# Optimization experiments

Measured on AMD Instinct MI355X. Metric: run time of the kernel, lower is better.

Reference implementation:

```python
import jax, jax.numpy as jnp
import numpy as np

DIM = 2048
N_HEADS = 32
N_KV_HEADS = 8
HEAD_DIM = 64
N_REP = N_HEADS // N_KV_HEADS
SEQ = 2048
BATCH = 1


def _llama3_scaled_rope(head_dim, end, base=10000.0, scale_factor=8):
    # matches executorch precompute_freqs_cis with use_scaled=True
    freqs = 1.0 / (base ** (np.arange(0, head_dim, 2)[: head_dim // 2] / head_dim))
    low_freq_factor, high_freq_factor, old_ctx = 1.0, 4.0, 8192.0
    low_wl = old_ctx / low_freq_factor
    high_wl = old_ctx / high_freq_factor
    wavelen = 2.0 * np.pi / freqs
    smooth = (old_ctx / wavelen - low_freq_factor) / (high_freq_factor - low_freq_factor)
    scaled = np.where(
        wavelen < high_wl,
        freqs,
        np.where(wavelen > low_wl, freqs / scale_factor,
                 (1.0 - smooth) * freqs / scale_factor + smooth * freqs),
    )
    t = np.arange(end, dtype=np.float64)
    ang = np.outer(t, scaled)
    return np.cos(ang).astype(np.float32), np.sin(ang).astype(np.float32)


def setup_inputs() -> dict:
    key = jax.random.key(0)
    kx, kq, kk, kv, ko = jax.random.split(key, 5)
    x = jax.random.normal(kx, (BATCH, SEQ, DIM), dtype=jnp.float32)
    sc = 0.02
    wq = jax.random.normal(kq, (N_HEADS * HEAD_DIM, DIM), dtype=jnp.float32) * sc
    wk = jax.random.normal(kk, (N_KV_HEADS * HEAD_DIM, DIM), dtype=jnp.float32) * sc
    wv = jax.random.normal(kv, (N_KV_HEADS * HEAD_DIM, DIM), dtype=jnp.float32) * sc
    wo = jax.random.normal(ko, (N_HEADS * HEAD_DIM, DIM), dtype=jnp.float32).T * sc
    cos, sin = _llama3_scaled_rope(HEAD_DIM, SEQ)
    return {"x": x, "freqs_cos": jnp.asarray(cos), "freqs_sin": jnp.asarray(sin),
            "wq": wq, "wk": wk, "wv": wv, "wo": wo}


def _apply_rotary(x, cos, sin):
    # x: [b, s, h, hd]; cos/sin: [s, hd//2]; interleaved-pair RoPE
    xr = x[..., 0::2]
    xi = x[..., 1::2]
    c = cos[None, :, None, :]
    s = sin[None, :, None, :]
    out_r = xr * c - xi * s
    out_i = xr * s + xi * c
    return jnp.stack([out_r, out_i], axis=-1).reshape(x.shape)


def reference(x, freqs_cos, freqs_sin, wq, wk, wv, wo):
    b, s, _ = x.shape
    q = (x @ wq.T).reshape(b, s, N_HEADS, HEAD_DIM)
    k = (x @ wk.T).reshape(b, s, N_KV_HEADS, HEAD_DIM)
    v = (x @ wv.T).reshape(b, s, N_KV_HEADS, HEAD_DIM)
    q = _apply_rotary(q, freqs_cos, freqs_sin)
    k = _apply_rotary(k, freqs_cos, freqs_sin)
    # [b, h, s, hd]
    q = q.transpose(0, 2, 1, 3)
    k = k.transpose(0, 2, 1, 3)
    v = v.transpose(0, 2, 1, 3)
    # GQA: repeat_interleave over head dim
    k = jnp.repeat(k, N_REP, axis=1)
    v = jnp.repeat(v, N_REP, axis=1)
    scale = 1.0 / jnp.sqrt(jnp.asarray(HEAD_DIM, dtype=x.dtype))
    scores = jnp.einsum("bhqd,bhkd->bhqk", q, k) * scale
    causal = jnp.tril(jnp.ones((s, s), dtype=bool))
    scores = jnp.where(causal[None, None], scores, jnp.finfo(scores.dtype).min)
    attn = jax.nn.softmax(scores, axis=-1)
    y = jnp.einsum("bhqk,bhkd->bhqd", attn, v)
    y = y.transpose(0, 2, 1, 3).reshape(b, s, N_HEADS * HEAD_DIM)
    return y @ wo.T
```

## Files before the change

kernel.cpp:

```cpp
#include <hip/hip_runtime.h>
#include <hip/hip_bf16.h>

typedef __attribute__((ext_vector_type(8))) __bf16 bf16x8;
typedef __attribute__((ext_vector_type(4))) __bf16 bf16x4;
typedef __attribute__((ext_vector_type(4))) float f32x4;
typedef __attribute__((ext_vector_type(16))) float f32x16;

#define DIM 2048
#define SEQ 2048
#define NH 32
#define NKV 8
#define HD 64
#define QKVD 3072
#define KOFF 2048
#define VOFF 2560
#define KVDIM 512

__device__ __forceinline__ void gld16(const __bf16* g, __bf16* l) {
    __builtin_amdgcn_global_load_lds(
        (const __attribute__((address_space(1))) void*)g,
        (__attribute__((address_space(3))) void*)l, 16, 0, 0);
}

__global__ __launch_bounds__(256) void cvt_all(const float* __restrict__ x,
                                               const float* __restrict__ wq,
                                               const float* __restrict__ wk,
                                               const float* __restrict__ wv,
                                               const float* __restrict__ wo,
                                               __bf16* __restrict__ xb,
                                               __bf16* __restrict__ wqkvb,
                                               __bf16* __restrict__ wob) {
    const int i = blockIdx.x * blockDim.x + threadIdx.x;
    const int NX = SEQ * DIM / 4;
    const int NW = DIM * DIM / 4;
    const int NKV4 = KVDIM * DIM / 4;
    const float* src; __bf16* dst; int off;
    if (i < NX)                        { src = x;  dst = xb;    off = i; }
    else if (i < NX + NW)              { src = wq; dst = wqkvb; off = i - NX; }
    else if (i < NX + NW + NKV4)       { src = wk; dst = wqkvb + (size_t)KOFF * DIM; off = i - NX - NW; }
    else if (i < NX + NW + 2 * NKV4)   { src = wv; dst = wqkvb + (size_t)VOFF * DIM; off = i - NX - NW - NKV4; }
    else                               { src = wo; dst = wob;   off = i - NX - NW - 2 * NKV4; }
    float4 v = reinterpret_cast<const float4*>(src)[off];
    bf16x4 o;
    o[0] = (__bf16)v.x; o[1] = (__bf16)v.y; o[2] = (__bf16)v.z; o[3] = (__bf16)v.w;
    reinterpret_cast<bf16x4*>(dst)[off] = o;
}

template <typename OutT, bool ROPE>
__global__ __launch_bounds__(512, 6) void gemm_tn(const __bf16* __restrict__ A,
                                                  const __bf16* __restrict__ B,
                                                  OutT* __restrict__ C,
                                                  int M, int N, int K,
                                                  float scale, int scaleNlim,
                                                  const float* __restrict__ fc,
                                                  const float* __restrict__ fs,
                                                  __bf16* __restrict__ VTout) {
    __shared__ __align__(16) __bf16 As[2][2][128 * 32];
    __shared__ __align__(16) __bf16 Bs[2][2][64 * 32];
    const int tid = threadIdx.x;
    const int lane = tid & 63;
    const int w = tid >> 6;
    const int l15 = lane & 15, lhi = lane >> 4;
    const int mb = blockIdx.y * 128;
    const int nb = blockIdx.x * 64;
    const int wm = (w >> 1) * 32, wn = (w & 1) * 32;

    const int srow = lane >> 2, scol = (lane & 3) * 8;
    const __bf16* gA = A + (size_t)(mb + w * 16 + srow) * K + scol;
    const __bf16* gB = B + (size_t)(nb + (w & 3) * 16 + srow) * K + scol;
    const int bsub = w >> 2;

    auto stage = [&](int kk, int buf) {
#pragma unroll
        for (int s = 0; s < 2; ++s)
            gld16(gA + kk + s * 32, As[buf][s] + w * 512);
        gld16(gB + kk + bsub * 32, Bs[buf][bsub] + (w & 3) * 512);
    };

    stage(0, 0);
    __syncthreads();

    f32x4 acc[2][2] = {};
    int cur = 0;
    for (int kk = 0; kk < K; kk += 64, cur ^= 1) {
        if (kk + 64 < K) stage(kk + 64, cur ^ 1);
#pragma unroll
        for (int s = 0; s < 2; ++s) {
            bf16x8 a[2], b[2];
#pragma unroll
            for (int i = 0; i < 2; ++i)
                a[i] = *reinterpret_cast<const bf16x8*>(&As[cur][s][(wm + i * 16 + l15) * 32 + lhi * 8]);
#pragma unroll
            for (int j = 0; j < 2; ++j)
                b[j] = *reinterpret_cast<const bf16x8*>(&Bs[cur][s][(wn + j * 16 + l15) * 32 + lhi * 8]);
#pragma unroll
            for (int i = 0; i < 2; ++i)
#pragma unroll
                for (int j = 0; j < 2; ++j)
                    acc[i][j] = __builtin_amdgcn_mfma_f32_16x16x32_bf16(a[i], b[j], acc[i][j], 0, 0, 0);
        }
        __syncthreads();
    }

    const bool toVT = ROPE && (VTout != nullptr) && (nb >= VOFF);
    if (toVT) {
#pragma unroll
        for (int i = 0; i < 2; ++i)
#pragma unroll
            for (int j = 0; j < 2; ++j) {
                bf16x4 pv;
#pragma unroll
                for (int r = 0; r < 4; ++r) pv[r] = (__bf16)acc[i][j][r];
                const int colv = nb - VOFF + wn + j * 16 + l15;
                const int row0 = mb + wm + i * 16 + lhi * 4;
                *reinterpret_cast<bf16x4*>(VTout + (size_t)colv * M + row0) = pv;
            }
    } else {
        const float sc = (nb < scaleNlim) ? scale : 1.0f;
        const bool doRope = ROPE && (nb < VOFF);
#pragma unroll
        for (int i = 0; i < 2; ++i)
#pragma unroll
            for (int j = 0; j < 2; ++j)
#pragma unroll
                for (int r = 0; r < 4; ++r) {
                    float v = acc[i][j][r] * sc;
                    if (doRope) {
                        const int col = nb + wn + j * 16 + l15;
                        const int row = mb + wm + i * 16 + lhi * 4 + r;
                        const float vp = __shfl_xor(v, 1);
                        const int fi = (col & 63) >> 1;
                        const float cc = fc[row * 32 + fi];
                        const float ss = fs[row * 32 + fi];
                        v = (col & 1) ? (vp * ss + v * cc) : (v * cc - vp * ss);
                    }
                    C[(size_t)(mb + wm + i * 16 + lhi * 4 + r) * N + nb + wn + j * 16 + l15] = (OutT)v;
                }
    }
}

__global__ __launch_bounds__(256, 4) void attn_kernel(const __bf16* __restrict__ QKV,
                                                      const __bf16* __restrict__ VT,
                                                      __bf16* __restrict__ Y) {
    const int bx = blockIdx.x;
    const int g = bx >> 8;
    const int a = (bx >> 5) & 7;
    const int h = bx & 31;
    const int qt = (g == 0) ? 31 - a : (g == 1) ? a : (g == 2) ? 23 - a : 8 + a;
    const int kvh = h >> 2;
    const int tid = threadIdx.x;
    const int lane = tid & 63;
    const int w = tid >> 6;
    const int l31 = lane & 31;
    const int lhi2 = lane >> 5;
    const int qhalf = w & 1;
    const int kvhalf = w >> 1;

    __shared__ __align__(16) unsigned char smem[40960];
    __bf16* Kl = (__bf16*)smem;
    __bf16* Vl = (__bf16*)(smem + 16384);
    __bf16* Pl = (__bf16*)(smem + 32768);

    const __bf16* Qp = QKV + h * HD;
    const __bf16* Kp = QKV + KOFF + kvh * HD;
    const __bf16* Vth = VT + (size_t)(kvh * HD) * SEQ;

    const int sr = lane >> 3;
    const int ksc = ((lane & 7) ^ sr) * 8;

    auto stage = [&](int jt, int buf) {
        const int kvb = jt * 64;
#pragma unroll
        for (int c = 0; c < 2; ++c) {
            const int row = w * 16 + c * 8;
            gld16(Kp + (size_t)(kvb + row + sr) * QKVD + ksc, Kl + buf * 4096 + row * 64);
            gld16(Vth + (size_t)(row + sr) * SEQ + kvb + ksc, Vl + buf * 4096 + row * 64);
        }
    };

    const int qb = qt * 64;
    const int qrow = qb + qhalf * 32 + l31;

    const __bf16* qptr = Qp + (size_t)qrow * QKVD;
    bf16x8 qf[4];
#pragma unroll
    for (int c = 0; c < 4; ++c)
        qf[c] = *reinterpret_cast<const bf16x8*>(qptr + c * 16 + lhi2 * 8);

    f32x16 o0 = {}, o1 = {};
    float mrun = -1e30f;
    float lpart = 0.f;

    const int pswz = l31 & 3;
    const int rsw7 = l31 & 7;

    stage(0, 0);
    __syncthreads();

    int cur = 0;
    for (int j = 0; j <= qt; ++j, cur ^= 1) {
        const bool pre = (j < qt);
        if (pre) stage(j + 1, cur ^ 1);

        if (!(j == qt && kvhalf == 1 && qhalf == 0)) {
            f32x16 sacc = {};
            const __bf16* Kb = Kl + cur * 4096 + (kvhalf * 32 + l31) * 64;
            __builtin_amdgcn_s_setprio(1);
#pragma unroll
            for (int c = 0; c < 4; ++c) {
                bf16x8 kf = *reinterpret_cast<const bf16x8*>(
                    Kb + (((c * 2 + lhi2) ^ rsw7) * 8));
                sacc = __builtin_amdgcn_mfma_f32_32x32x16_bf16(kf, qf[c], sacc, 0, 0, 0);
            }
            __builtin_amdgcn_s_setprio(0);

            if (j == qt && kvhalf == qhalf) {
#pragma unroll
                for (int r = 0; r < 16; ++r) {
                    const int kvl = (r & 3) + 8 * (r >> 2) + 4 * lhi2;
                    if (kvl > l31) sacc[r] = -1e30f;
                }
            }

            float pm = sacc[0];
#pragma unroll
            for (int r = 1; r < 16; ++r) pm = fmaxf(pm, sacc[r]);

            if (!__all(pm - mrun <= 8.0f)) {
                const float full = fmaxf(pm, __shfl_xor(pm, 32));
                const float mn = fmaxf(mrun, full);
                const float aa = exp2f(mrun - mn);
                mrun = mn;
                lpart *= aa;
#pragma unroll
                for (int r = 0; r < 16; ++r) {
                    const int qi = (r & 3) + 8 * (r >> 2) + 4 * lhi2;
                    const float ar = __shfl(aa, qi);
                    o0[r] *= ar; o1[r] *= ar;
                }
            }

            __bf16* Pw = Pl + w * 1024 + l31 * 32;
            float ps = 0.f;
#pragma unroll
            for (int gg = 0; gg < 4; ++gg) {
                bf16x4 pk;
#pragma unroll
                for (int rr = 0; rr < 4; ++rr) {
                    const float pv = exp2f(sacc[gg * 4 + rr] - mrun);
                    ps += pv;
                    pk[rr] = (__bf16)pv;
                }
                *reinterpret_cast<bf16x4*>(Pw + ((gg ^ pswz) * 8) + lhi2 * 4) = pk;
            }
            lpart += ps;

            bf16x8 pf[2];
#pragma unroll
            for (int c = 0; c < 2; ++c)
                pf[c] = *reinterpret_cast<const bf16x8*>(
                    Pw + (((c * 2 + lhi2) ^ pswz) * 8));
            const __bf16* Vb0 = Vl + cur * 4096 + l31 * 64;
            const __bf16* Vb1 = Vl + cur * 4096 + (32 + l31) * 64;
            __builtin_amdgcn_s_setprio(1);
#pragma unroll
            for (int c = 0; c < 2; ++c) {
                const int s = kvhalf * 4 + c * 2 + lhi2;
                bf16x8 vf0 = *reinterpret_cast<const bf16x8*>(Vb0 + ((s ^ rsw7) * 8));
                bf16x8 vf1 = *reinterpret_cast<const bf16x8*>(Vb1 + ((s ^ rsw7) * 8));
                o0 = __builtin_amdgcn_mfma_f32_32x32x16_bf16(pf[c], vf0, o0, 0, 0, 0);
                o1 = __builtin_amdgcn_mfma_f32_32x32x16_bf16(pf[c], vf1, o1, 0, 0, 0);
            }
            __builtin_amdgcn_s_setprio(0);
        }

        __syncthreads();
    }

    const float ls = lpart + __shfl_xor(lpart, 32);
    float* ex = (float*)smem;
    float* exm = (float*)(smem + 32768);

    if (kvhalf == 1) {
        float* dst = ex + qhalf * 2048 + lane * 32;
#pragma unroll
        for (int r = 0; r < 16; ++r) { dst[r] = o0[r]; dst[16 + r] = o1[r]; }
        if (lane < 32) {
            exm[qhalf * 64 + l31] = mrun;
            exm[qhalf * 64 + 32 + l31] = ls;
        }
    }
    __syncthreads();
    if (kvhalf == 0) {
        const float mo = exm[qhalf * 64 + l31];
        const float lso = exm[qhalf * 64 + 32 + l31];
        const float mn = fmaxf(mrun, mo);
        const float a0 = exp2f(mrun - mn);
        const float a1 = exp2f(mo - mn);
        const float lst = ls * a0 + lso * a1;
        const float* src = ex + qhalf * 2048 + lane * 32;
#pragma unroll
        for (int r = 0; r < 16; ++r) {
            const int qi = (r & 3) + 8 * (r >> 2) + 4 * lhi2;
            const float A0 = __shfl(a0, qi);
            const float A1 = __shfl(a1, qi);
            const float L = __shfl(lst, qi);
            const float v0 = (o0[r] * A0 + src[r] * A1) / L;
            const float v1 = (o1[r] * A0 + src[16 + r] * A1) / L;
            const size_t qg = (size_t)(qb + qhalf * 32 + qi);
            Y[qg * DIM + h * HD + l31] = (__bf16)v0;
            Y[qg * DIM + h * HD + 32 + l31] = (__bf16)v1;
        }
    }
}

extern "C" void kernel_launch(void* const* d_in, const int* in_sizes, int n_in,
                              void* d_out, int out_size, void* d_ws, size_t ws_size,
                              hipStream_t stream) {
    const float* x    = (const float*)d_in[0];
    const float* fcos = (const float*)d_in[1];
    const float* fsin = (const float*)d_in[2];
    const float* wq   = (const float*)d_in[3];
    const float* wk   = (const float*)d_in[4];
    const float* wv   = (const float*)d_in[5];
    const float* wo   = (const float*)d_in[6];
    float* out = (float*)d_out;

    __bf16* xb    = (__bf16*)d_ws;
    __bf16* wqkvb = xb + (size_t)SEQ * DIM;
    __bf16* wob   = wqkvb + (size_t)QKVD * DIM;
    __bf16* QKVb  = wob + (size_t)DIM * DIM;
    __bf16* Yb    = QKVb + (size_t)SEQ * QKVD;
    __bf16* VTb   = Yb + (size_t)SEQ * DIM;

    const int ncvt = (SEQ * DIM / 4) + 2 * (DIM * DIM / 4) + 2 * (KVDIM * DIM / 4);
    cvt_all<<<ncvt / 256, 256, 0, stream>>>(x, wq, wk, wv, wo, xb, wqkvb, wob);

    gemm_tn<__bf16, true><<<dim3(QKVD / 64, SEQ / 128), 512, 0, stream>>>(
        xb, wqkvb, QKVb, SEQ, QKVD, DIM, 0.125f * 1.4426950408889634f, KOFF,
        fcos, fsin, VTb);

    attn_kernel<<<dim3(1024), 256, 0, stream>>>(QKVb, VTb, Yb);

    gemm_tn<float, false><<<dim3(DIM / 64, SEQ / 128), 512, 0, stream>>>(
        Yb, wob, out, SEQ, DIM, DIM, 1.0f, 0, nullptr, nullptr, nullptr);
}
```

Baseline: 132.2 us.

## Process two query tiles per attention block and keep P in registers via permlane swap

The attention kernel now runs 512 threads per block covering two adjacent 64-row query tiles, so each staged K/V tile is shared by twice as many waves and the grid is halved. The PV MFMA operands are swapped so the probability fragment can be built in registers with packed bf16 conversion and permlane32_swap instead of a round trip through LDS. This drops per-row rescale shuffles and vectorizes the output stores. The cost is more threads per block, uneven causal work between the two tiles, and a changed block-to-tile mapping for load balance.

```diff
diff --git a/kernel.cpp b/kernel.cpp
--- a/kernel.cpp
+++ b/kernel.cpp
@@ -5,6 +5,7 @@
 typedef __attribute__((ext_vector_type(4))) __bf16 bf16x4;
 typedef __attribute__((ext_vector_type(4))) float f32x4;
 typedef __attribute__((ext_vector_type(16))) float f32x16;
+typedef __attribute__((ext_vector_type(4))) unsigned u32x4;
 
 #define DIM 2048
 #define SEQ 2048
@@ -20,6 +21,12 @@
     __builtin_amdgcn_global_load_lds(
         (const __attribute__((address_space(1))) void*)g,
         (__attribute__((address_space(3))) void*)l, 16, 0, 0);
+}
+
+__device__ __forceinline__ unsigned cvtpk(float lo, float hi) {
+    unsigned r;
+    asm("v_cvt_pk_bf16_f32 %0, %1, %2" : "=v"(r) : "v"(lo), "v"(hi));
+    return r;
 }
 
 __global__ __launch_bounds__(256) void cvt_all(const float* __restrict__ x,
@@ -139,27 +146,26 @@
     }
 }
 
-__global__ __launch_bounds__(256, 4) void attn_kernel(const __bf16* __restrict__ QKV,
+__global__ __launch_bounds__(512, 4) void attn_kernel(const __bf16* __restrict__ QKV,
                                                       const __bf16* __restrict__ VT,
                                                       __bf16* __restrict__ Y) {
     const int bx = blockIdx.x;
     const int g = bx >> 8;
     const int a = (bx >> 5) & 7;
     const int h = bx & 31;
-    const int qt = (g == 0) ? 31 - a : (g == 1) ? a : (g == 2) ? 23 - a : 8 + a;
+    const int p = g ? a : 15 - a;
     const int kvh = h >> 2;
     const int tid = threadIdx.x;
     const int lane = tid & 63;
     const int w = tid >> 6;
+    const int qtl = w >> 2, qhalf = w & 1, kvhalf = (w >> 1) & 1;
     const int l31 = lane & 31;
     const int lhi2 = lane >> 5;
-    const int qhalf = w & 1;
-    const int kvhalf = w >> 1;
-
-    __shared__ __align__(16) unsigned char smem[40960];
-    __bf16* Kl = (__bf16*)smem;
-    __bf16* Vl = (__bf16*)(smem + 16384);
-    __bf16* Pl = (__bf16*)(smem + 32768);
+
+    __shared__ __align__(16) __bf16 Kl[2][64 * 64];
+    __shared__ __align__(16) __bf16 Vl[2][64 * 64];
+    __shared__ float ex[4][64][32];
+    __shared__ float exm[4][2][32];
 
     const __bf16* Qp = QKV + h * HD;
     const __bf16* Kp = QKV + KOFF + kvh * HD;
@@ -170,16 +176,12 @@
 
     auto stage = [&](int jt, int buf) {
         const int kvb = jt * 64;
-#pragma unroll
-        for (int c = 0; c < 2; ++c) {
-            const int row = w * 16 + c * 8;
-            gld16(Kp + (size_t)(kvb + row + sr) * QKVD + ksc, Kl + buf * 4096 + row * 64);
-            gld16(Vth + (size_t)(row + sr) * SEQ + kvb + ksc, Vl + buf * 4096 + row * 64);
-        }
+        gld16(Kp + (size_t)(kvb + w * 8 + sr) * QKVD + ksc, &Kl[buf][w * 512]);
+        gld16(Vth + (size_t)(w * 8 + sr) * SEQ + kvb + ksc, &Vl[buf][w * 512]);
     };
 
-    const int qb = qt * 64;
-    const int qrow = qb + qhalf * 32 + l31;
+    const int qb = (2 * p + qtl) * 64 + qhalf * 32;
+    const int qrow = qb + l31;
 
     const __bf16* qptr = Qp + (size_t)qrow * QKVD;
     bf16x8 qf[4];
@@ -190,21 +192,20 @@
     f32x16 o0 = {}, o1 = {};
     float mrun = -1e30f;
     float lpart = 0.f;
-
-    const int pswz = l31 & 3;
     const int rsw7 = l31 & 7;
 
+    const int nj = 2 * p + 2;
     stage(0, 0);
     __syncthreads();
 
     int cur = 0;
-    for (int j = 0; j <= qt; ++j, cur ^= 1) {
-        const bool pre = (j < qt);
-        if (pre) stage(j + 1, cur ^ 1);
-
-        if (!(j == qt && kvhalf == 1 && qhalf == 0)) {
+    for (int j = 0; j < nj; ++j, cur ^= 1) {
+        if (j + 1 < nj) stage(j + 1, cur ^ 1);
+
+        const int kvmin = j * 64 + kvhalf * 32;
+        if (kvmin <= qb + 31) {
             f32x16 sacc = {};
-            const __bf16* Kb = Kl + cur * 4096 + (kvhalf * 32 + l31) * 64;
+            const __bf16* Kb = &Kl[cur][(kvhalf * 32 + l31) * 64];
             __builtin_amdgcn_s_setprio(1);
 #pragma unroll
             for (int c = 0; c < 4; ++c) {
@@ -214,62 +215,57 @@
             }
             __builtin_amdgcn_s_setprio(0);
 
-            if (j == qt && kvhalf == qhalf) {
+            if (kvmin + 31 > qb) {
 #pragma unroll
                 for (int r = 0; r < 16; ++r) {
-                    const int kvl = (r & 3) + 8 * (r >> 2) + 4 * lhi2;
-                    if (kvl > l31) sacc[r] = -1e30f;
+                    const int kv = kvmin + (r & 3) + 8 * (r >> 2) + 4 * lhi2;
+                    if (kv > qrow) sacc[r] = -1e30f;
                 }
             }
 
             float pm = sacc[0];
 #pragma unroll
             for (int r = 1; r < 16; ++r) pm = fmaxf(pm, sacc[r]);
+            pm = fmaxf(pm, __shfl_xor(pm, 32));
 
             if (!__all(pm - mrun <= 8.0f)) {
-                const float full = fmaxf(pm, __shfl_xor(pm, 32));
-                const float mn = fmaxf(mrun, full);
+                const float mn = fmaxf(mrun, pm);
                 const float aa = exp2f(mrun - mn);
                 mrun = mn;
                 lpart *= aa;
 #pragma unroll
-                for (int r = 0; r < 16; ++r) {
-                    const int qi = (r & 3) + 8 * (r >> 2) + 4 * lhi2;
-                    const float ar = __shfl(aa, qi);
-                    o0[r] *= ar; o1[r] *= ar;
+                for (int r = 0; r < 16; ++r) { o0[r] *= aa; o1[r] *= aa; }
+            }
+
+            unsigned pk[4][2];
+            float ps = 0.f;
+#pragma unroll
+            for (int g4 = 0; g4 < 4; ++g4) {
+                float pv[4];
+#pragma unroll
+                for (int i = 0; i < 4; ++i) {
+                    pv[i] = exp2f(sacc[g4 * 4 + i] - mrun);
+                    ps += pv[i];
                 }
-            }
-
-            __bf16* Pw = Pl + w * 1024 + l31 * 32;
-            float ps = 0.f;
-#pragma unroll
-            for (int gg = 0; gg < 4; ++gg) {
-                bf16x4 pk;
-#pragma unroll
-                for (int rr = 0; rr < 4; ++rr) {
-                    const float pv = exp2f(sacc[gg * 4 + rr] - mrun);
-                    ps += pv;
-                    pk[rr] = (__bf16)pv;
-                }
-                *reinterpret_cast<bf16x4*>(Pw + ((gg ^ pswz) * 8) + lhi2 * 4) = pk;
+                pk[g4][0] = cvtpk(pv[0], pv[1]);
+                pk[g4][1] = cvtpk(pv[2], pv[3]);
             }
             lpart += ps;
 
-            bf16x8 pf[2];
-#pragma unroll
-            for (int c = 0; c < 2; ++c)
-                pf[c] = *reinterpret_cast<const bf16x8*>(
-                    Pw + (((c * 2 + lhi2) ^ pswz) * 8));
-            const __bf16* Vb0 = Vl + cur * 4096 + l31 * 64;
-            const __bf16* Vb1 = Vl + cur * 4096 + (32 + l31) * 64;
+            const __bf16* Vb0 = &Vl[cur][l31 * 64];
+            const __bf16* Vb1 = &Vl[cur][(32 + l31) * 64];
             __builtin_amdgcn_s_setprio(1);
 #pragma unroll
             for (int c = 0; c < 2; ++c) {
+                auto sw0 = __builtin_amdgcn_permlane32_swap(pk[2 * c][0], pk[2 * c + 1][0], false, false);
+                auto sw1 = __builtin_amdgcn_permlane32_swap(pk[2 * c][1], pk[2 * c + 1][1], false, false);
+                u32x4 fw = {sw0[0], sw1[0], sw0[1], sw1[1]};
+                bf16x8 pf = __builtin_bit_cast(bf16x8, fw);
                 const int s = kvhalf * 4 + c * 2 + lhi2;
                 bf16x8 vf0 = *reinterpret_cast<const bf16x8*>(Vb0 + ((s ^ rsw7) * 8));
                 bf16x8 vf1 = *reinterpret_cast<const bf16x8*>(Vb1 + ((s ^ rsw7) * 8));
-                o0 = __builtin_amdgcn_mfma_f32_32x32x16_bf16(pf[c], vf0, o0, 0, 0, 0);
-                o1 = __builtin_amdgcn_mfma_f32_32x32x16_bf16(pf[c], vf1, o1, 0, 0, 0);
+                o0 = __builtin_amdgcn_mfma_f32_32x32x16_bf16(vf0, pf, o0, 0, 0, 0);
+                o1 = __builtin_amdgcn_mfma_f32_32x32x16_bf16(vf1, pf, o1, 0, 0, 0);
             }
             __builtin_amdgcn_s_setprio(0);
         }
@@ -278,38 +274,36 @@
     }
 
     const float ls = lpart + __shfl_xor(lpart, 32);
-    float* ex = (float*)smem;
-    float* exm = (float*)(smem + 32768);
-
-    if (kvhalf == 1) {
-        float* dst = ex + qhalf * 2048 + lane * 32;
+    const int reg = qtl * 2 + qhalf;
+
+    if (kvhalf) {
+        float* dst = &ex[reg][lane][0];
 #pragma unroll
         for (int r = 0; r < 16; ++r) { dst[r] = o0[r]; dst[16 + r] = o1[r]; }
-        if (lane < 32) {
-            exm[qhalf * 64 + l31] = mrun;
-            exm[qhalf * 64 + 32 + l31] = ls;
-        }
+        if (lane < 32) { exm[reg][0][l31] = mrun; exm[reg][1][l31] = ls; }
     }
     __syncthreads();
-    if (kvhalf == 0) {
-        const float mo = exm[qhalf * 64 + l31];
-        const float lso = exm[qhalf * 64 + 32 + l31];
+    if (!kvhalf) {
+        const float mo = exm[reg][0][l31];
+        const float lso = exm[reg][1][l31];
         const float mn = fmaxf(mrun, mo);
-        const float a0 = exp2f(mrun - mn);
-        const float a1 = exp2f(mo - mn);
-        const float lst = ls * a0 + lso * a1;
-        const float* src = ex + qhalf * 2048 + lane * 32;
-#pragma unroll
-        for (int r = 0; r < 16; ++r) {
-            const int qi = (r & 3) + 8 * (r >> 2) + 4 * lhi2;
-            const float A0 = __shfl(a0, qi);
-            const float A1 = __shfl(a1, qi);
-            const float L = __shfl(lst, qi);
-            const float v0 = (o0[r] * A0 + src[r] * A1) / L;
-            const float v1 = (o1[r] * A0 + src[16 + r] * A1) / L;
-            const size_t qg = (size_t)(qb + qhalf * 32 + qi);
-            Y[qg * DIM + h * HD + l31] = (__bf16)v0;
-            Y[qg * DIM + h * HD + 32 + l31] = (__bf16)v1;
+        const float A0 = exp2f(mrun - mn);
+        const float A1 = exp2f(mo - mn);
+        const float L = ls * A0 + lso * A1;
+        const float* src = &ex[reg][lane][0];
+        const size_t ybase = (size_t)qrow * DIM + h * HD;
+#pragma unroll
+        for (int g4 = 0; g4 < 4; ++g4) {
+            bf16x4 y0, y1;
+#pragma unroll
+            for (int i = 0; i < 4; ++i) {
+                const int r = g4 * 4 + i;
+                y0[i] = (__bf16)((o0[r] * A0 + src[r] * A1) / L);
+                y1[i] = (__bf16)((o1[r] * A0 + src[16 + r] * A1) / L);
+            }
+            const int d0 = 8 * g4 + 4 * lhi2;
+            *reinterpret_cast<bf16x4*>(Y + ybase + d0) = y0;
+            *reinterpret_cast<bf16x4*>(Y + ybase + 32 + d0) = y1;
         }
     }
 }
@@ -340,7 +334,7 @@
         xb, wqkvb, QKVb, SEQ, QKVD, DIM, 0.125f * 1.4426950408889634f, KOFF,
         fcos, fsin, VTb);
 
-    attn_kernel<<<dim3(1024), 256, 0, stream>>>(QKVb, VTb, Yb);
+    attn_kernel<<<dim3(512), 512, 0, stream>>>(QKVb, VTb, Yb);
 
     gemm_tn<float, false><<<dim3(DIM / 64, SEQ / 128), 512, 0, stream>>>(
         Yb, wob, out, SEQ, DIM, DIM, 1.0f, 0, nullptr, nullptr, nullptr);
```

After: 136.9 us. +3.6%, slower.
